# Performance work log

Measured on AMD Instinct MI355X. Metric: run time of the kernel, lower is better.

## Reference

```python
import jax, jax.numpy as jnp
import numpy as np

EMB = 1024  # embedding_size in the torch module


def setup_inputs() -> dict:
    key = jax.random.key(0)
    ks = jax.random.split(key, 6)
    B, N, K = 64, 256, 4096
    y = jax.random.normal(ks[0], (B, N, 1024), dtype=jnp.float32)
    # nn.Linear weights, init normal(std=0.02), zero bias
    Wy_w = jax.random.normal(ks[1], (1024, 1024), dtype=jnp.float32) * 0.02  # [out,in]
    Wy_b = jnp.zeros((1024,), dtype=jnp.float32)
    Wz_w = jax.random.normal(ks[2], (1024, 2048), dtype=jnp.float32) * 0.02  # [out,in]
    Wz_b = jnp.zeros((1024,), dtype=jnp.float32)
    dic_z = jax.random.normal(ks[3], (K, 2048), dtype=jnp.float32)
    prior = jax.random.uniform(ks[4], (K,), dtype=jnp.float32)
    prior = prior / jnp.sum(prior)
    return {"y": y, "Wy_w": Wy_w, "Wy_b": Wy_b, "Wz_w": Wz_w, "Wz_b": Wz_b,
            "dic_z": dic_z, "prior": prior}


def reference(y, Wy_w, Wy_b, Wz_w, Wz_b, dic_z, prior):
    # h = Wy(y): [B,N,1024]; dz = Wz(dic_z): [K,1024]
    h = jnp.einsum('bni,oi->bno', y, Wy_w) + Wy_b
    dz = jnp.einsum('ki,oi->ko', dic_z, Wz_w) + Wz_b
    # attention over dictionary: [B,N,K]
    att = jax.nn.softmax(jnp.einsum('bnd,kd->bnk', h, dz) / jnp.sqrt(jnp.float32(EMB)), axis=-1)
    # z[b,n] = sum_k prior[k] * att[b,n,k] * dic_z[k]  -> [B,N,2048]
    # (avoids the [B,N,K,2048] intermediate the torch code materializes)
    z = jnp.einsum('bnk,k,ke->bne', att, prior, dic_z)
    return z
```

## Files before the change

kernel.cpp:

```cpp
#include <hip/hip_runtime.h>
#include <hip/hip_bf16.h>
#include <stdint.h>

typedef __bf16 bf16;
typedef __bf16 bf16x4 __attribute__((ext_vector_type(4)));
typedef __bf16 bf16x8 __attribute__((ext_vector_type(8)));
typedef float f32x4 __attribute__((ext_vector_type(4)));
typedef unsigned short ushort8 __attribute__((ext_vector_type(8)));

__device__ __forceinline__ void gload16(const bf16* g, char* l) {
  __builtin_amdgcn_global_load_lds(
      reinterpret_cast<const __attribute__((address_space(1))) unsigned int*>(
          reinterpret_cast<uintptr_t>(g)),
      reinterpret_cast<__attribute__((address_space(3))) unsigned int*>(
          reinterpret_cast<uintptr_t>(l)),
      16, 0, 0);
}

#define VMCNT(n) asm volatile("s_waitcnt vmcnt(" #n ")" ::: "memory")

__global__ __launch_bounds__(256) void cast_bf16(const float* __restrict__ in,
                                                 bf16* __restrict__ out, int n8) {
  int i = blockIdx.x * blockDim.x + threadIdx.x;
  const int stride = gridDim.x * blockDim.x;
  for (; i < n8; i += stride) {
    const float4 v0 = reinterpret_cast<const float4*>(in)[i * 2];
    const float4 v1 = reinterpret_cast<const float4*>(in)[i * 2 + 1];
    bf16x8 o = { (bf16)v0.x, (bf16)v0.y, (bf16)v0.z, (bf16)v0.w,
                 (bf16)v1.x, (bf16)v1.y, (bf16)v1.z, (bf16)v1.w };
    reinterpret_cast<bf16x8*>(out)[i] = o;
  }
}

template <bool OUT_BF16, bool HAS_BIAS, int BN>
__global__ __launch_bounds__(512, 2) void gemm_pipe(
    const bf16* __restrict__ A, const bf16* __restrict__ B,
    const float* __restrict__ bias, void* __restrict__ Cout,
    int M, int N, int K, float scale) {
  constexpr int BM = 256;
  constexpr int SLOT = (BM + BN) * 64;
  constexpr int BOFF = BM * 64;
  constexpr int TM = (BN == 256) ? 128 : 64;
  constexpr int MI = TM / 16;
  constexpr int NI = 4;
  extern __shared__ char lds[];
  const int tid = threadIdx.x;
  const int lane = tid & 63, w = tid >> 6;

  const int gridN = N / BN;
  const int nwg = gridDim.x;
  const int orig = blockIdx.x;
  int wgid;
  { const int q = nwg >> 3, r = nwg & 7, x = orig & 7, rest = orig >> 3;
    wgid = (x < r ? x * (q + 1) : r * (q + 1) + (x - r) * q) + rest; }
  const int m0 = (wgid / gridN) * BM;
  const int n0 = (wgid % gridN) * BN;

  const int srow = w * 16 + (lane >> 2);
  const int scol = (((lane & 3) ^ ((srow >> 1) & 3))) * 8;
  const bf16* gA  = A + (size_t)(m0 + srow) * K + scol;
  const bf16* gA2 = gA + (size_t)128 * K;
  const bf16* gB  = B + (size_t)(n0 + srow) * K + scol;
  const bf16* gB2 = (BN == 256) ? gB + (size_t)128 * K : gB;

  auto stage = [&](int T) {
    char* sb = lds + (size_t)(T & 3) * SLOT;
    const int kc = T * 32;
    gload16(gA + kc,  sb + w * 1024);
    gload16(gA2 + kc, sb + 8192 + w * 1024);
    gload16(gB + kc,  sb + BOFF + w * 1024);
    if constexpr (BN == 256) gload16(gB2 + kc, sb + BOFF + 8192 + w * 1024);
  };

  const int fr = lane & 15, hi = lane >> 4;
  int wm, wn;
  if constexpr (BN == 256) { wm = w >> 2; wn = w & 3; }
  else                     { wm = w >> 1; wn = w & 1; }
  const int arow = wm * TM + fr;
  const int aoff0 = arow * 64 + ((hi ^ ((arow >> 1) & 3)) << 4);
  const int brow = wn * 64 + fr;
  const int boff0 = BOFF + brow * 64 + ((hi ^ ((brow >> 1) & 3)) << 4);

  f32x4 acc[MI][NI] = {};
  const int NT = K >> 5;

  stage(0); stage(1); stage(2);
  if constexpr (BN == 256) VMCNT(8); else VMCNT(6);
  __builtin_amdgcn_s_barrier();

  for (int t = 0; t < NT; ++t) {
    const char* sb = lds + (size_t)(t & 3) * SLOT;
    bf16x8 af[MI], bb[NI];
    af[0] = *(const bf16x8*)(sb + aoff0);
#pragma unroll
    for (int i = 0; i < NI; ++i) bb[i] = *(const bf16x8*)(sb + boff0 + i * 1024);
#pragma unroll
    for (int i = 1; i < MI; ++i) af[i] = *(const bf16x8*)(sb + aoff0 + i * 1024);
    if (t + 3 < NT) stage(t + 3);
    __builtin_amdgcn_s_barrier();
    __builtin_amdgcn_s_setprio(1);
#pragma unroll
    for (int mi = 0; mi < MI; ++mi)
#pragma unroll
      for (int ni = 0; ni < NI; ++ni)
        acc[mi][ni] = __builtin_amdgcn_mfma_f32_16x16x32_bf16(af[mi], bb[ni], acc[mi][ni], 0, 0, 0);
    __builtin_amdgcn_s_setprio(0);
    if (t + 3 < NT) {
      if constexpr (BN == 256) VMCNT(8); else VMCNT(6);
    } else if (t + 2 < NT) {
      if constexpr (BN == 256) VMCNT(4); else VMCNT(3);
    } else if (t + 1 < NT) {
      VMCNT(0);
    }
    __builtin_amdgcn_s_barrier();
  }

  const int lro = hi * 4;
#pragma unroll
  for (int ni = 0; ni < NI; ++ni) {
    const int gcol = n0 + wn * 64 + ni * 16 + fr;
    float bvs = 0.f;
    if constexpr (HAS_BIAS) bvs = bias[gcol];
#pragma unroll
    for (int mi = 0; mi < MI; ++mi) {
      const int grow = m0 + wm * TM + mi * 16 + lro;
#pragma unroll
      for (int j = 0; j < 4; ++j) {
        const float c = acc[mi][ni][j] * scale + bvs;
        if constexpr (OUT_BF16)
          ((bf16*)Cout)[(size_t)(grow + j) * N + gcol] = (bf16)c;
        else
          ((float*)Cout)[(size_t)(grow + j) * N + gcol] = c;
      }
    }
  }
}

__global__ __launch_bounds__(256) void prep_w3t(const float* __restrict__ dic,
                                                const float* __restrict__ prior,
                                                bf16* __restrict__ w3t) {
  const int KD = 4096, E = 2048;
  __shared__ bf16 t[64][72];
  const int k0 = blockIdx.x * 64, e0 = blockIdx.y * 64;
  const int tid = threadIdx.x;
  const int er = (tid & 15) * 4;
  const int kr = tid >> 4;
#pragma unroll
  for (int p = 0; p < 4; ++p) {
    const int k = kr + p * 16;
    const float pr = prior[k0 + k];
    const float4 v = *reinterpret_cast<const float4*>(dic + (size_t)(k0 + k) * E + e0 + er);
    t[er + 0][k] = (bf16)(v.x * pr);
    t[er + 1][k] = (bf16)(v.y * pr);
    t[er + 2][k] = (bf16)(v.z * pr);
    t[er + 3][k] = (bf16)(v.w * pr);
  }
  __syncthreads();
  const int e = tid >> 2, kc = (tid & 3) * 16;
  ushort8 a = *reinterpret_cast<ushort8*>(&t[e][kc]);
  ushort8 b = *reinterpret_cast<ushort8*>(&t[e][kc + 8]);
  unsigned short* dst = (unsigned short*)w3t + (size_t)(e0 + e) * KD + k0 + kc;
  *reinterpret_cast<ushort8*>(dst) = a;
  *reinterpret_cast<ushort8*>(dst + 8) = b;
}

__global__ __launch_bounds__(256) void softmax_rows(unsigned short* __restrict__ S) {
  const int K = 4096;
  unsigned short* row = S + (size_t)blockIdx.x * K;
  const int tid = threadIdx.x;
  const int lane = tid & 63, w = tid >> 6;
  __shared__ float red[8];

  ushort8 v0 = *reinterpret_cast<const ushort8*>(row + tid * 8);
  ushort8 v1 = *reinterpret_cast<const ushort8*>(row + 2048 + tid * 8);
  float x[16];
#pragma unroll
  for (int i = 0; i < 8; ++i) {
    x[i]     = __uint_as_float(((unsigned)v0[i]) << 16);
    x[8 + i] = __uint_as_float(((unsigned)v1[i]) << 16);
  }
  float mx = x[0];
#pragma unroll
  for (int i = 1; i < 16; ++i) mx = fmaxf(mx, x[i]);
#pragma unroll
  for (int o = 32; o; o >>= 1) mx = fmaxf(mx, __shfl_xor(mx, o));
  if (lane == 0) red[w] = mx;
  __syncthreads();
  mx = fmaxf(fmaxf(red[0], red[1]), fmaxf(red[2], red[3]));

  float s = 0.f;
#pragma unroll
  for (int i = 0; i < 16; ++i) { x[i] = __expf(x[i] - mx); s += x[i]; }
#pragma unroll
  for (int o = 32; o; o >>= 1) s += __shfl_xor(s, o);
  if (lane == 0) red[4 + w] = s;
  __syncthreads();
  const float inv = 1.f / (red[4] + red[5] + red[6] + red[7]);

  ushort8 o0, o1;
#pragma unroll
  for (int i = 0; i < 8; ++i) {
    bf16 b0 = (bf16)(x[i] * inv);
    bf16 b1 = (bf16)(x[8 + i] * inv);
    o0[i] = __builtin_bit_cast(unsigned short, b0);
    o1[i] = __builtin_bit_cast(unsigned short, b1);
  }
  *reinterpret_cast<ushort8*>(row + tid * 8) = o0;
  *reinterpret_cast<ushort8*>(row + 2048 + tid * 8) = o1;
}

extern "C" void kernel_launch(void* const* d_in, const int* in_sizes, int n_in,
                              void* d_out, int out_size, void* d_ws, size_t ws_size,
                              hipStream_t stream) {
  const float* y     = (const float*)d_in[0];
  const float* Wy_w  = (const float*)d_in[1];
  const float* Wy_b  = (const float*)d_in[2];
  const float* Wz_w  = (const float*)d_in[3];
  const float* Wz_b  = (const float*)d_in[4];
  const float* dic   = (const float*)d_in[5];
  const float* prior = (const float*)d_in[6];
  float* z = (float*)d_out;

  const int M = 16384, D = 1024, E = 2048, KD = 4096;

  char* ws = (char*)d_ws;
  bf16* w3t  = (bf16*)(ws);
  bf16* h    = (bf16*)(ws + ((size_t)16 << 20));
  bf16* dzb  = (bf16*)(ws + ((size_t)48 << 20));
  bf16* S    = (bf16*)(ws + ((size_t)56 << 20));
  bf16* yb   = (bf16*)(ws + ((size_t)56 << 20));
  bf16* Wyb  = (bf16*)(ws + ((size_t)88 << 20));
  bf16* Wzb  = (bf16*)(ws + ((size_t)90 << 20));
  bf16* dicb = (bf16*)(ws + ((size_t)94 << 20));

  cast_bf16<<<2048, 256, 0, stream>>>(y, yb, M * D / 8);
  cast_bf16<<<512, 256, 0, stream>>>(Wy_w, Wyb, D * D / 8);
  cast_bf16<<<512, 256, 0, stream>>>(Wz_w, Wzb, D * E / 8);
  cast_bf16<<<1024, 256, 0, stream>>>(dic, dicb, KD * E / 8);
  prep_w3t<<<dim3(KD / 64, E / 64), 256, 0, stream>>>(dic, prior, w3t);
  gemm_pipe<true, true, 256><<<(M / 256) * (D / 256), 512, 131072, stream>>>(
      yb, Wyb, Wy_b, h, M, D, D, 1.0f);
  gemm_pipe<true, true, 128><<<(KD / 256) * (D / 128), 512, 98304, stream>>>(
      dicb, Wzb, Wz_b, dzb, KD, D, E, 1.0f);
  gemm_pipe<true, false, 256><<<(M / 256) * (KD / 256), 512, 131072, stream>>>(
      h, dzb, nullptr, S, M, KD, D, 0.03125f);
  softmax_rows<<<M, 256, 0, stream>>>((unsigned short*)S);
  gemm_pipe<false, false, 256><<<(M / 256) * (E / 256), 512, 131072, stream>>>(
      S, w3t, nullptr, z, M, E, KD, 1.0f);
}
```

Baseline: 574.2 us.

## Split GEMM k-step into two MFMA phases interleaving A/B prefetch

For the BN=256 path, each k-iteration is split into two halves. The first half computes the upper four M fragments while the A tile for t+3 is issued. The second half computes the lower four M fragments while the B tile is issued, so global-to-LDS loads are spread across two MFMA bursts and fewer fragment registers are live at once. Explicit lgkmcnt(0) waits with sched_barrier are added before the MFMA blocks, and the BN=128 path now fixes MI at 4. This adds an extra barrier per iteration, and the ordering constraints may limit compiler scheduling.

```diff
diff --git a/kernel.cpp b/kernel.cpp
--- a/kernel.cpp
+++ b/kernel.cpp
@@ -18,6 +18,8 @@
 }
 
 #define VMCNT(n) asm volatile("s_waitcnt vmcnt(" #n ")" ::: "memory")
+#define LGKM0()  do { asm volatile("s_waitcnt lgkmcnt(0)" ::: "memory"); \
+                      __builtin_amdgcn_sched_barrier(0); } while (0)
 
 __global__ __launch_bounds__(256) void cast_bf16(const float* __restrict__ in,
                                                  bf16* __restrict__ out, int n8) {
@@ -63,11 +65,15 @@
   const bf16* gB  = B + (size_t)(n0 + srow) * K + scol;
   const bf16* gB2 = (BN == 256) ? gB + (size_t)128 * K : gB;
 
-  auto stage = [&](int T) {
+  auto stageA = [&](int T) {
     char* sb = lds + (size_t)(T & 3) * SLOT;
     const int kc = T * 32;
     gload16(gA + kc,  sb + w * 1024);
     gload16(gA2 + kc, sb + 8192 + w * 1024);
+  };
+  auto stageB = [&](int T) {
+    char* sb = lds + (size_t)(T & 3) * SLOT;
+    const int kc = T * 32;
     gload16(gB + kc,  sb + BOFF + w * 1024);
     if constexpr (BN == 256) gload16(gB2 + kc, sb + BOFF + 8192 + w * 1024);
   };
@@ -84,35 +90,67 @@
   f32x4 acc[MI][NI] = {};
   const int NT = K >> 5;
 
-  stage(0); stage(1); stage(2);
+  stageA(0); stageB(0); stageA(1); stageB(1); stageA(2); stageB(2);
   if constexpr (BN == 256) VMCNT(8); else VMCNT(6);
   __builtin_amdgcn_s_barrier();
 
   for (int t = 0; t < NT; ++t) {
     const char* sb = lds + (size_t)(t & 3) * SLOT;
-    bf16x8 af[MI], bb[NI];
-    af[0] = *(const bf16x8*)(sb + aoff0);
-#pragma unroll
-    for (int i = 0; i < NI; ++i) bb[i] = *(const bf16x8*)(sb + boff0 + i * 1024);
-#pragma unroll
-    for (int i = 1; i < MI; ++i) af[i] = *(const bf16x8*)(sb + aoff0 + i * 1024);
-    if (t + 3 < NT) stage(t + 3);
-    __builtin_amdgcn_s_barrier();
-    __builtin_amdgcn_s_setprio(1);
-#pragma unroll
-    for (int mi = 0; mi < MI; ++mi)
-#pragma unroll
-      for (int ni = 0; ni < NI; ++ni)
-        acc[mi][ni] = __builtin_amdgcn_mfma_f32_16x16x32_bf16(af[mi], bb[ni], acc[mi][ni], 0, 0, 0);
-    __builtin_amdgcn_s_setprio(0);
-    if (t + 3 < NT) {
-      if constexpr (BN == 256) VMCNT(8); else VMCNT(6);
-    } else if (t + 2 < NT) {
-      if constexpr (BN == 256) VMCNT(4); else VMCNT(3);
-    } else if (t + 1 < NT) {
-      VMCNT(0);
+    bf16x8 af[4], bb[NI];
+
+    if constexpr (BN == 256) {
+#pragma unroll
+      for (int i = 0; i < NI; ++i) bb[i] = *(const bf16x8*)(sb + boff0 + i * 1024);
+#pragma unroll
+      for (int i = 0; i < 4; ++i) af[i] = *(const bf16x8*)(sb + aoff0 + i * 1024);
+      if (t + 3 < NT) stageA(t + 3);
+      __builtin_amdgcn_s_barrier();
+      LGKM0();
+      __builtin_amdgcn_s_setprio(1);
+#pragma unroll
+      for (int mi = 0; mi < 4; ++mi)
+#pragma unroll
+        for (int ni = 0; ni < NI; ++ni)
+          acc[mi][ni] = __builtin_amdgcn_mfma_f32_16x16x32_bf16(af[mi], bb[ni], acc[mi][ni], 0, 0, 0);
+      __builtin_amdgcn_s_setprio(0);
+      __builtin_amdgcn_s_barrier();
+#pragma unroll
+      for (int i = 0; i < 4; ++i) af[i] = *(const bf16x8*)(sb + aoff0 + (4 + i) * 1024);
+      if (t + 3 < NT) stageB(t + 3);
+      __builtin_amdgcn_s_barrier();
+      LGKM0();
+      __builtin_amdgcn_s_setprio(1);
+#pragma unroll
+      for (int mi = 0; mi < 4; ++mi)
+#pragma unroll
+        for (int ni = 0; ni < NI; ++ni)
+          acc[4 + mi][ni] = __builtin_amdgcn_mfma_f32_16x16x32_bf16(af[mi], bb[ni], acc[4 + mi][ni], 0, 0, 0);
+      __builtin_amdgcn_s_setprio(0);
+      if (t + 3 < NT)      VMCNT(8);
+      else if (t + 2 < NT) VMCNT(4);
+      else if (t + 1 < NT) VMCNT(0);
+      __builtin_amdgcn_s_barrier();
+    } else {
+      af[0] = *(const bf16x8*)(sb + aoff0);
+#pragma unroll
+      for (int i = 0; i < NI; ++i) bb[i] = *(const bf16x8*)(sb + boff0 + i * 1024);
+#pragma unroll
+      for (int i = 1; i < 4; ++i) af[i] = *(const bf16x8*)(sb + aoff0 + i * 1024);
+      if (t + 3 < NT) { stageA(t + 3); stageB(t + 3); }
+      __builtin_amdgcn_s_barrier();
+      LGKM0();
+      __builtin_amdgcn_s_setprio(1);
+#pragma unroll
+      for (int mi = 0; mi < 4; ++mi)
+#pragma unroll
+        for (int ni = 0; ni < NI; ++ni)
+          acc[mi][ni] = __builtin_amdgcn_mfma_f32_16x16x32_bf16(af[mi], bb[ni], acc[mi][ni], 0, 0, 0);
+      __builtin_amdgcn_s_setprio(0);
+      if (t + 3 < NT)      VMCNT(6);
+      else if (t + 2 < NT) VMCNT(3);
+      else if (t + 1 < NT) VMCNT(0);
+      __builtin_amdgcn_s_barrier();
     }
-    __builtin_amdgcn_s_barrier();
   }
 
   const int lro = hi * 4;
```

New measurement: 576.9 us. Within noise of the previous version (+0.5%).
